# Kernel optimization log

Measured on AMD Instinct MI355X. Metric: run time of the kernel, lower is better.

## Reference

```python
import jax, jax.numpy as jnp
import numpy as np

DIM_CAP = 16   # capsule dim
NCLS = 17      # annotation_nr
BS = 16
T = 120        # chunk_size * fps
P = 22         # players per frame graph
G = BS * T     # number of graphs = 1920
N = G * P      # nodes = 42240
C_IN = 14
CHS = [16, 32, 64, 152]  # 8m,16m,32m,76m with m=2
BN_EPS = 1e-3


def _build_graph():
    # fully-connected directed edges within each 22-node graph (no self loops)
    ii, jj = np.meshgrid(np.arange(P), np.arange(P), indexing='ij')
    mask = ii != jj
    li, lj = ii[mask], jj[mask]               # (462,)
    base = (np.arange(G) * P)[:, None]
    src = (base + li[None, :]).reshape(-1)
    dst = (base + lj[None, :]).reshape(-1)
    edge_index = np.stack([src, dst]).astype(np.int64)   # (2, E)
    batch = np.repeat(np.arange(G), P).astype(np.int64)  # (N,)
    return jnp.asarray(edge_index), jnp.asarray(batch)


def setup_inputs() -> dict:
    key = jax.random.key(0)
    ks = jax.random.split(key, 16)
    edge_index, batch = _build_graph()
    E = edge_index.shape[1]
    x = jax.random.normal(ks[0], (N, C_IN), dtype=jnp.float32)
    edge_attr = jax.random.uniform(ks[1], (E, 5), dtype=jnp.float32)
    dims = [C_IN] + CHS
    params = {}
    for i in range(4):
        s = 1.0 / np.sqrt(dims[i])
        params[f'W{i+1}'] = jax.random.normal(ks[2 + i], (dims[i], dims[i + 1]), dtype=jnp.float32) * s
        params[f'b{i+1}'] = jnp.zeros((dims[i + 1],), dtype=jnp.float32)
    c_out = DIM_CAP * NCLS  # 272
    params['conv_w'] = jax.random.normal(ks[6], (c_out, CHS[-1], 3), dtype=jnp.float32) * (1.0 / np.sqrt(CHS[-1] * 3))
    params['conv_b'] = jnp.zeros((c_out,), dtype=jnp.float32)
    params['bn_gamma'] = jnp.ones((T,), dtype=jnp.float32)
    params['bn_beta'] = jnp.zeros((T,), dtype=jnp.float32)
    return dict(x=x, edge_index=edge_index, batch=batch, edge_attr=edge_attr, **params)


def _gcn_layer(x, src, dst, w_edge, W, b):
    # PyG GCNConv: x' = D^-1/2 (A + I) D^-1/2 (x W) + b, edge weights w, self-loop weight 1
    n = x.shape[0]
    h = x @ W
    loop = jnp.arange(n)
    src_f = jnp.concatenate([src, loop])
    dst_f = jnp.concatenate([dst, loop])
    w_f = jnp.concatenate([w_edge, jnp.ones((n,), h.dtype)])
    deg = jax.ops.segment_sum(w_f, dst_f, num_segments=n)
    dinv = jnp.where(deg > 0, jax.lax.rsqrt(deg), 0.0)
    norm = dinv[src_f] * w_f * dinv[dst_f]
    out = jax.ops.segment_sum(norm[:, None] * h[src_f], dst_f, num_segments=n)
    return out + b


def reference(x, edge_index, batch, edge_attr, W1, b1, W2, b2, W3, b3, W4, b4,
              conv_w, conv_b, bn_gamma, bn_beta):
    src, dst = edge_index[0], edge_index[1]
    ew = edge_attr[:, 4]
    h = jax.nn.relu(_gcn_layer(x, src, dst, ew, W1, b1))
    h = jax.nn.relu(_gcn_layer(h, src, dst, ew, W2, b2))
    h = jax.nn.relu(_gcn_layer(h, src, dst, ew, W3, b3))
    h = jax.nn.relu(_gcn_layer(h, src, dst, ew, W4, b4))
    # global mean pool per graph -> (G, 152)
    ones = jnp.ones((h.shape[0],), h.dtype)
    cnt = jax.ops.segment_sum(ones, batch, num_segments=G)
    pooled = jax.ops.segment_sum(h, batch, num_segments=G) / jnp.clip(cnt, 1.0)[:, None]
    # (BS, T, 152) -> (BS, 152, T); conv kernel (3,1) with pad (1,1) on T
    feat = pooled.reshape(BS, T, CHS[-1]).transpose(0, 2, 1)
    conv = jax.lax.conv_general_dilated(
        feat, conv_w, window_strides=(1,), padding=[(1, 1)],
        dimension_numbers=('NCH', 'OIH', 'NCH'))
    conv = conv + conv_b[None, :, None]            # (BS, 272, T)
    caps = conv.transpose(0, 2, 1).reshape(BS, T, DIM_CAP, NCLS)
    # BatchNorm2d(num_features=T) in eval mode: running mean 0, var 1
    scale = (bn_gamma / jnp.sqrt(1.0 + BN_EPS))[None, :, None, None]
    shift = bn_beta[None, :, None, None]
    s = jax.nn.sigmoid(caps * scale + shift)
    out = jnp.sqrt(jnp.sum(jnp.square(s - 0.5), axis=2) * 4.0 / DIM_CAP)
    return out  # (BS, T, NCLS)
```

## Files before the change

### kernel.cpp

```cpp
#include <hip/hip_runtime.h>
#include <hip/hip_bf16.h>

#define GROUPS 1920
#define CH4 152
#define BUFS 100

template<int DIN, int KR>
__device__ __forceinline__ void layerA(const float* buf, float* Ut,
                                       const float* A4, int tid)
{
    constexpr int NKT = DIN / KR;
    constexpr int NT = NKT * 12;
    if (tid < NT) {
        const int kt = tid / 12, pt = tid - kt * 12;
        const int g = pt / 3, ps = (pt - g * 3) * 8;
        const int col0 = g * 24 + ps;
        const int xcol = g * 24;
        float acc[KR][8];
        #pragma unroll
        for (int j = 0; j < KR; ++j)
            #pragma unroll
            for (int a = 0; a < 8; ++a) acc[j][a] = 0.f;
        #pragma unroll 2
        for (int q = 0; q < 22; ++q) {
            const float4 a0 = *(const float4*)(A4 + (q * 4 + g) * 28 + ps);
            const float4 a1 = *(const float4*)(A4 + (q * 4 + g) * 28 + ps + 4);
            float xv[KR];
            #pragma unroll
            for (int j = 0; j < KR; ++j) xv[j] = buf[(kt * KR + j) * BUFS + xcol + q];
            #pragma unroll
            for (int j = 0; j < KR; ++j) {
                acc[j][0] = fmaf(xv[j], a0.x, acc[j][0]);
                acc[j][1] = fmaf(xv[j], a0.y, acc[j][1]);
                acc[j][2] = fmaf(xv[j], a0.z, acc[j][2]);
                acc[j][3] = fmaf(xv[j], a0.w, acc[j][3]);
                acc[j][4] = fmaf(xv[j], a1.x, acc[j][4]);
                acc[j][5] = fmaf(xv[j], a1.y, acc[j][5]);
                acc[j][6] = fmaf(xv[j], a1.z, acc[j][6]);
                acc[j][7] = fmaf(xv[j], a1.w, acc[j][7]);
            }
        }
        #pragma unroll
        for (int j = 0; j < KR; ++j) {
            *(float4*)(Ut + (kt * KR + j) * BUFS + col0) =
                make_float4(acc[j][0], acc[j][1], acc[j][2], acc[j][3]);
            *(float4*)(Ut + (kt * KR + j) * BUFS + col0 + 4) =
                make_float4(acc[j][4], acc[j][5], acc[j][6], acc[j][7]);
        }
    }
}

template<int DIN, int DOUT, int CR>
__device__ __forceinline__ void layerB(const float* __restrict__ W,
                                       const float* __restrict__ B,
                                       const float* Ut, float* buf, int tid)
{
    constexpr int NCT = DOUT / CR;
    constexpr int NT = NCT * 12;
    if (tid < NT) {
        const int ct = tid / 12, pt = tid - ct * 12;
        const int p0 = pt * 8, c0 = ct * CR;
        float acc[CR][8];
        #pragma unroll
        for (int b = 0; b < CR; ++b) {
            const float bias = B[c0 + b];
            #pragma unroll
            for (int a = 0; a < 8; ++a) acc[b][a] = bias;
        }
        #pragma unroll 4
        for (int k = 0; k < DIN; ++k) {
            const float4 u0 = *(const float4*)(Ut + k * BUFS + p0);
            const float4 u1 = *(const float4*)(Ut + k * BUFS + p0 + 4);
            float wv[CR];
            #pragma unroll
            for (int b = 0; b < CR; b += 4) {
                const float4 w4 = *(const float4*)(W + k * DOUT + c0 + b);
                wv[b] = w4.x; wv[b + 1] = w4.y; wv[b + 2] = w4.z; wv[b + 3] = w4.w;
            }
            #pragma unroll
            for (int b = 0; b < CR; ++b) {
                acc[b][0] = fmaf(wv[b], u0.x, acc[b][0]);
                acc[b][1] = fmaf(wv[b], u0.y, acc[b][1]);
                acc[b][2] = fmaf(wv[b], u0.z, acc[b][2]);
                acc[b][3] = fmaf(wv[b], u0.w, acc[b][3]);
                acc[b][4] = fmaf(wv[b], u1.x, acc[b][4]);
                acc[b][5] = fmaf(wv[b], u1.y, acc[b][5]);
                acc[b][6] = fmaf(wv[b], u1.z, acc[b][6]);
                acc[b][7] = fmaf(wv[b], u1.w, acc[b][7]);
            }
        }
        #pragma unroll
        for (int b = 0; b < CR; ++b) {
            *(float4*)(buf + (c0 + b) * BUFS + p0) =
                make_float4(fmaxf(acc[b][0], 0.f), fmaxf(acc[b][1], 0.f),
                            fmaxf(acc[b][2], 0.f), fmaxf(acc[b][3], 0.f));
            *(float4*)(buf + (c0 + b) * BUFS + p0 + 4) =
                make_float4(fmaxf(acc[b][4], 0.f), fmaxf(acc[b][5], 0.f),
                            fmaxf(acc[b][6], 0.f), fmaxf(acc[b][7], 0.f));
        }
    }
}

__global__ __launch_bounds__(256) void gcn_kernel(
    const float* __restrict__ x, const float* __restrict__ ea,
    const float* __restrict__ W1, const float* __restrict__ b1,
    const float* __restrict__ W2, const float* __restrict__ b2,
    const float* __restrict__ W3, const float* __restrict__ b3,
    const float* __restrict__ W4, const float* __restrict__ b4,
    float* __restrict__ pooledT)
{
    __shared__ __align__(16) float A4[24 * 4 * 28];
    __shared__ __align__(16) float dv[4 * 24];
    __shared__ __align__(16) float buf[64 * BUFS];
    __shared__ __align__(16) float Ut[64 * BUFS];

    const int tid = threadIdx.x;
    const int G0 = blockIdx.x * 4;

    for (int idx = tid; idx < 24 * 4 * 28; idx += 256) {
        const int q = idx / 112, r = idx - q * 112;
        const int g = r / 28, p = r - g * 28;
        float v = 0.f;
        if (q < 22 && p < 22) {
            if (q == p) v = 1.0f;
            else {
                const int e = q * 21 + p - (p > q);
                v = ea[((size_t)(G0 + g) * 462 + e) * 5 + 4];
            }
        }
        A4[idx] = v;
    }
    for (int idx = tid; idx < 14 * 96; idx += 256) {
        const int k = idx / 96, col = idx - k * 96;
        const int g = col / 24, p = col - g * 24;
        buf[k * BUFS + col] = (p < 22) ? x[((size_t)(G0 + g) * 22 + p) * 14 + k] : 0.f;
    }
    __syncthreads();

    if (tid < 96) {
        const int g = tid / 24, p = tid - g * 24;
        float s = 0.f;
        #pragma unroll
        for (int q = 0; q < 22; ++q) s += A4[(q * 4 + g) * 28 + p];
        dv[tid] = (s > 0.f) ? rsqrtf(s) : 0.f;
    }
    __syncthreads();
    for (int idx = tid; idx < 24 * 4 * 28; idx += 256) {
        const int q = idx / 112, r = idx - q * 112;
        const int g = r / 28, p = r - g * 28;
        if (p < 24) A4[idx] *= dv[g * 24 + q] * dv[g * 24 + p];
    }
    __syncthreads();

    layerA<14, 2>(buf, Ut, A4, tid);  __syncthreads();
    layerB<14, 16, 4>(W1, b1, Ut, buf, tid);  __syncthreads();
    layerA<16, 4>(buf, Ut, A4, tid);  __syncthreads();
    layerB<16, 32, 4>(W2, b2, Ut, buf, tid);  __syncthreads();
    layerA<32, 4>(buf, Ut, A4, tid);  __syncthreads();
    layerB<32, 64, 8>(W3, b3, Ut, buf, tid);  __syncthreads();
    layerA<64, 4>(buf, Ut, A4, tid);  __syncthreads();

    float* pscr = buf;
    if (tid < 19 * 12) {
        const int ct = tid / 12, pt = tid - ct * 12;
        const int p0 = pt * 8, c0 = ct * 8;
        float acc[8][8];
        #pragma unroll
        for (int b = 0; b < 8; ++b) {
            const float bias = b4[c0 + b];
            #pragma unroll
            for (int a = 0; a < 8; ++a) acc[b][a] = bias;
        }
        #pragma unroll 4
        for (int k = 0; k < 64; ++k) {
            const float4 u0 = *(const float4*)(Ut + k * BUFS + p0);
            const float4 u1 = *(const float4*)(Ut + k * BUFS + p0 + 4);
            float wv[8];
            #pragma unroll
            for (int b = 0; b < 8; b += 4) {
                const float4 w4 = *(const float4*)(W4 + k * 152 + c0 + b);
                wv[b] = w4.x; wv[b + 1] = w4.y; wv[b + 2] = w4.z; wv[b + 3] = w4.w;
            }
            #pragma unroll
            for (int b = 0; b < 8; ++b) {
                acc[b][0] = fmaf(wv[b], u0.x, acc[b][0]);
                acc[b][1] = fmaf(wv[b], u0.y, acc[b][1]);
                acc[b][2] = fmaf(wv[b], u0.z, acc[b][2]);
                acc[b][3] = fmaf(wv[b], u0.w, acc[b][3]);
                acc[b][4] = fmaf(wv[b], u1.x, acc[b][4]);
                acc[b][5] = fmaf(wv[b], u1.y, acc[b][5]);
                acc[b][6] = fmaf(wv[b], u1.z, acc[b][6]);
                acc[b][7] = fmaf(wv[b], u1.w, acc[b][7]);
            }
        }
        const int alim = ((pt % 3) == 2) ? 6 : 8;
        float ps8[8];
        #pragma unroll
        for (int b = 0; b < 8; ++b) {
            float s = 0.f;
            #pragma unroll
            for (int a = 0; a < 8; ++a)
                s += (a < alim) ? fmaxf(acc[b][a], 0.f) : 0.f;
            ps8[b] = s;
        }
        *(float4*)(pscr + pt * 152 + c0) = make_float4(ps8[0], ps8[1], ps8[2], ps8[3]);
        *(float4*)(pscr + pt * 152 + c0 + 4) = make_float4(ps8[4], ps8[5], ps8[6], ps8[7]);
    }
    __syncthreads();

    if (tid < 152) {
        const int c = tid;
        const int b = G0 / 120, t0 = G0 - b * 120;
        float4 v;
        #pragma unroll
        for (int g = 0; g < 4; ++g) {
            const float s = pscr[(g * 3 + 0) * 152 + c] + pscr[(g * 3 + 1) * 152 + c]
                          + pscr[(g * 3 + 2) * 152 + c];
            ((float*)&v)[g] = s * (1.0f / 22.0f);
        }
        *(float4*)(pooledT + ((size_t)(b * 152 + c) * 128) + 4 + t0) = v;
    }
}

__global__ __launch_bounds__(256) void repack_conv_w(const float* __restrict__ cw,
                                                     float* __restrict__ wT,
                                                     float* __restrict__ pT)
{
    const int idx = blockIdx.x * 256 + threadIdx.x;
    if (idx < 272 * 456) {
        const int o = idx / 456, r = idx - o * 456;
        wT[r * 272 + o] = cw[idx];
    } else {
        const int j = idx - 272 * 456;
        if (j < 16 * 152 * 8) {
            const int row = j >> 3, s = j & 7;
            const int slot = (s < 4) ? s : s + 120;
            pT[(size_t)row * 128 + slot] = 0.f;
        }
    }
}

__global__ __launch_bounds__(320) void conv_caps_kernel(
    const float* __restrict__ pT, const float* __restrict__ wT,
    const float* __restrict__ cb, const float* __restrict__ gamma,
    const float* __restrict__ beta, float* __restrict__ out)
{
    __shared__ __align__(16) float s2[8 * 272];
    __shared__ float sc[8], sh[8];

    const int bx = blockIdx.x;
    const int b = bx / 15, tile = bx - b * 15;
    const int t0 = tile * 8;
    const int tid = threadIdx.x;

    if (tid < 8) {
        const int t = t0 + tid;
        sc[tid] = gamma[t] * 0.999500374688f;
        sh[tid] = beta[t];
    }
    __syncthreads();

    if (tid < 272) {
        const int o = tid;
        const float cb0 = cb[o];
        float acc[8];
        #pragma unroll
        for (int tt = 0; tt < 8; ++tt) acc[tt] = cb0;
        const float* wp0 = wT + o;
        const float* frow0 = pT + ((size_t)b * 152) * 128 + 3 + t0;
        float w0 = wp0[0], w1 = wp0[272], w2 = wp0[544];
        #pragma unroll 2
        for (int i = 0; i < CH4; ++i) {
            const int inext = (i == CH4 - 1) ? i : i + 1;
            const float* nwp = wp0 + inext * 816;
            const float nw0 = nwp[0], nw1 = nwp[272], nw2 = nwp[544];
            const float* f = frow0 + (size_t)i * 128;
            float fr[10];
            #pragma unroll
            for (int j = 0; j < 10; ++j) fr[j] = f[j];
            #pragma unroll
            for (int tt = 0; tt < 8; ++tt)
                acc[tt] = fmaf(w0, fr[tt], fmaf(w1, fr[tt + 1], fmaf(w2, fr[tt + 2], acc[tt])));
            w0 = nw0; w1 = nw1; w2 = nw2;
        }
        #pragma unroll
        for (int tt = 0; tt < 8; ++tt) {
            const float z = fmaf(acc[tt], sc[tt], sh[tt]);
            const float s = 1.0f / (1.0f + __expf(-z));
            const float d = s - 0.5f;
            s2[tt * 272 + o] = d * d;
        }
    }
    __syncthreads();

    for (int e = tid; e < 8 * 17; e += 320) {
        const int tt = e / 17, n = e - tt * 17;
        float s = 0.f;
        #pragma unroll
        for (int d = 0; d < 16; ++d) s += s2[tt * 272 + d * 17 + n];
        out[((size_t)b * 120 + t0 + tt) * 17 + n] = sqrtf(s) * 0.5f;
    }
}

extern "C" void kernel_launch(void* const* d_in, const int* in_sizes, int n_in,
                              void* d_out, int out_size, void* d_ws, size_t ws_size,
                              hipStream_t stream) {
    const float* x     = (const float*)d_in[0];
    const float* ea    = (const float*)d_in[3];
    const float* W1    = (const float*)d_in[4];
    const float* b1    = (const float*)d_in[5];
    const float* W2    = (const float*)d_in[6];
    const float* b2    = (const float*)d_in[7];
    const float* W3    = (const float*)d_in[8];
    const float* b3    = (const float*)d_in[9];
    const float* W4    = (const float*)d_in[10];
    const float* b4    = (const float*)d_in[11];
    const float* cw    = (const float*)d_in[12];
    const float* cb    = (const float*)d_in[13];
    const float* gamma = (const float*)d_in[14];
    const float* beta  = (const float*)d_in[15];
    float* out = (float*)d_out;

    float* pT = (float*)d_ws;
    float* wT = pT + (size_t)16 * 152 * 128;

    hipLaunchKernelGGL(repack_conv_w, dim3((272 * 456 + 16 * 152 * 8 + 255) / 256),
                       dim3(256), 0, stream, cw, wT, pT);
    hipLaunchKernelGGL(gcn_kernel, dim3(GROUPS / 4), dim3(256), 0, stream,
                       x, ea, W1, b1, W2, b2, W3, b3, W4, b4, pT);
    hipLaunchKernelGGL(conv_caps_kernel, dim3(16 * 15), dim3(320), 0, stream,
                       pT, wT, cb, gamma, beta, out);
}
```

Measured before the change: 168.9 us.

## Process one graph per 64-thread block with XOR-swizzled shared layout

The GCN kernel now handles one graph per block of 64 threads (1920 blocks) instead of four graphs per 256-thread block (480 blocks). Shared-memory tiles shrink to 32-wide rows with an XOR swizzle meant to avoid bank conflicts, and per-thread register tiles are retuned (smaller KR/CR). The aim is more blocks for better occupancy and load balance across CUs, fewer idle threads, and less LDS per block. The trade-offs are less reuse of weight loads across graphs, scalar rather than float4 pooled writes, and more launch and setup work spread over more blocks.

New measurement: 172.2 us. No clear change (+1.9%).

```diff
diff --git a/kernel.cpp b/kernel.cpp
--- a/kernel.cpp
+++ b/kernel.cpp
@@ -3,19 +3,23 @@
 
 #define GROUPS 1920
 #define CH4 152
-#define BUFS 100
+
+__device__ __forceinline__ int rh(int r) { return (r + (r >> 3)) & 7; }
+__device__ __forceinline__ int swz(int r, int c) {
+    return (r << 5) + ((((c >> 2) ^ rh(r)) << 2) | (c & 3));
+}
+__device__ __forceinline__ int swz4(int r, int c4) {
+    return (r << 5) + ((c4 ^ rh(r)) << 2);
+}
 
 template<int DIN, int KR>
 __device__ __forceinline__ void layerA(const float* buf, float* Ut,
-                                       const float* A4, int tid)
-{
-    constexpr int NKT = DIN / KR;
-    constexpr int NT = NKT * 12;
+                                       const float* A, int tid)
+{
+    constexpr int NT = (DIN / KR) * 3;
     if (tid < NT) {
-        const int kt = tid / 12, pt = tid - kt * 12;
-        const int g = pt / 3, ps = (pt - g * 3) * 8;
-        const int col0 = g * 24 + ps;
-        const int xcol = g * 24;
+        const int kt = tid / 3, pt = tid - kt * 3;
+        const int p0 = pt * 8;
         float acc[KR][8];
         #pragma unroll
         for (int j = 0; j < KR; ++j)
@@ -23,11 +27,11 @@
             for (int a = 0; a < 8; ++a) acc[j][a] = 0.f;
         #pragma unroll 2
         for (int q = 0; q < 22; ++q) {
-            const float4 a0 = *(const float4*)(A4 + (q * 4 + g) * 28 + ps);
-            const float4 a1 = *(const float4*)(A4 + (q * 4 + g) * 28 + ps + 4);
+            const float4 a0 = *(const float4*)(A + q * 28 + p0);
+            const float4 a1 = *(const float4*)(A + q * 28 + p0 + 4);
             float xv[KR];
             #pragma unroll
-            for (int j = 0; j < KR; ++j) xv[j] = buf[(kt * KR + j) * BUFS + xcol + q];
+            for (int j = 0; j < KR; ++j) xv[j] = buf[swz(kt * KR + j, q)];
             #pragma unroll
             for (int j = 0; j < KR; ++j) {
                 acc[j][0] = fmaf(xv[j], a0.x, acc[j][0]);
@@ -42,9 +46,10 @@
         }
         #pragma unroll
         for (int j = 0; j < KR; ++j) {
-            *(float4*)(Ut + (kt * KR + j) * BUFS + col0) =
+            const int k = kt * KR + j;
+            *(float4*)(Ut + swz4(k, pt * 2)) =
                 make_float4(acc[j][0], acc[j][1], acc[j][2], acc[j][3]);
-            *(float4*)(Ut + (kt * KR + j) * BUFS + col0 + 4) =
+            *(float4*)(Ut + swz4(k, pt * 2 + 1)) =
                 make_float4(acc[j][4], acc[j][5], acc[j][6], acc[j][7]);
         }
     }
@@ -52,30 +57,36 @@
 
 template<int DIN, int DOUT, int CR>
 __device__ __forceinline__ void layerB(const float* __restrict__ W,
-                                       const float* __restrict__ B,
+                                       const float* __restrict__ Bb,
                                        const float* Ut, float* buf, int tid)
 {
-    constexpr int NCT = DOUT / CR;
-    constexpr int NT = NCT * 12;
+    constexpr int NT = (DOUT / CR) * 3;
     if (tid < NT) {
-        const int ct = tid / 12, pt = tid - ct * 12;
-        const int p0 = pt * 8, c0 = ct * CR;
+        const int ct = tid / 3, pt = tid - ct * 3;
+        const int c0 = ct * CR;
         float acc[CR][8];
         #pragma unroll
         for (int b = 0; b < CR; ++b) {
-            const float bias = B[c0 + b];
+            const float bias = Bb[c0 + b];
             #pragma unroll
             for (int a = 0; a < 8; ++a) acc[b][a] = bias;
         }
-        #pragma unroll 4
+        #pragma unroll 2
         for (int k = 0; k < DIN; ++k) {
-            const float4 u0 = *(const float4*)(Ut + k * BUFS + p0);
-            const float4 u1 = *(const float4*)(Ut + k * BUFS + p0 + 4);
+            const float4 u0 = *(const float4*)(Ut + swz4(k, pt * 2));
+            const float4 u1 = *(const float4*)(Ut + swz4(k, pt * 2 + 1));
             float wv[CR];
-            #pragma unroll
-            for (int b = 0; b < CR; b += 4) {
-                const float4 w4 = *(const float4*)(W + k * DOUT + c0 + b);
-                wv[b] = w4.x; wv[b + 1] = w4.y; wv[b + 2] = w4.z; wv[b + 3] = w4.w;
+            if constexpr (CR == 1) {
+                wv[0] = W[k * DOUT + c0];
+            } else if constexpr (CR == 2) {
+                const float2 w2 = *(const float2*)(W + k * DOUT + c0);
+                wv[0] = w2.x; wv[1] = w2.y;
+            } else {
+                #pragma unroll
+                for (int b = 0; b < CR; b += 4) {
+                    const float4 w4 = *(const float4*)(W + k * DOUT + c0 + b);
+                    wv[b] = w4.x; wv[b + 1] = w4.y; wv[b + 2] = w4.z; wv[b + 3] = w4.w;
+                }
             }
             #pragma unroll
             for (int b = 0; b < CR; ++b) {
@@ -91,17 +102,18 @@
         }
         #pragma unroll
         for (int b = 0; b < CR; ++b) {
-            *(float4*)(buf + (c0 + b) * BUFS + p0) =
+            const int r = c0 + b;
+            *(float4*)(buf + swz4(r, pt * 2)) =
                 make_float4(fmaxf(acc[b][0], 0.f), fmaxf(acc[b][1], 0.f),
                             fmaxf(acc[b][2], 0.f), fmaxf(acc[b][3], 0.f));
-            *(float4*)(buf + (c0 + b) * BUFS + p0 + 4) =
+            *(float4*)(buf + swz4(r, pt * 2 + 1)) =
                 make_float4(fmaxf(acc[b][4], 0.f), fmaxf(acc[b][5], 0.f),
                             fmaxf(acc[b][6], 0.f), fmaxf(acc[b][7], 0.f));
         }
     }
 }
 
-__global__ __launch_bounds__(256) void gcn_kernel(
+__global__ __launch_bounds__(64) void gcn_kernel(
     const float* __restrict__ x, const float* __restrict__ ea,
     const float* __restrict__ W1, const float* __restrict__ b1,
     const float* __restrict__ W2, const float* __restrict__ b2,
@@ -109,61 +121,58 @@
     const float* __restrict__ W4, const float* __restrict__ b4,
     float* __restrict__ pooledT)
 {
-    __shared__ __align__(16) float A4[24 * 4 * 28];
-    __shared__ __align__(16) float dv[4 * 24];
-    __shared__ __align__(16) float buf[64 * BUFS];
-    __shared__ __align__(16) float Ut[64 * BUFS];
+    __shared__ __align__(16) float sA[24 * 28];
+    __shared__ float dv[24];
+    __shared__ __align__(16) float buf[64 * 32];
+    __shared__ __align__(16) float Ut[64 * 32];
 
     const int tid = threadIdx.x;
-    const int G0 = blockIdx.x * 4;
-
-    for (int idx = tid; idx < 24 * 4 * 28; idx += 256) {
-        const int q = idx / 112, r = idx - q * 112;
-        const int g = r / 28, p = r - g * 28;
+    const int g = blockIdx.x;
+
+    for (int idx = tid; idx < 24 * 28; idx += 64) {
+        const int q = idx / 28, p = idx - q * 28;
         float v = 0.f;
         if (q < 22 && p < 22) {
             if (q == p) v = 1.0f;
             else {
                 const int e = q * 21 + p - (p > q);
-                v = ea[((size_t)(G0 + g) * 462 + e) * 5 + 4];
-            }
-        }
-        A4[idx] = v;
-    }
-    for (int idx = tid; idx < 14 * 96; idx += 256) {
-        const int k = idx / 96, col = idx - k * 96;
-        const int g = col / 24, p = col - g * 24;
-        buf[k * BUFS + col] = (p < 22) ? x[((size_t)(G0 + g) * 22 + p) * 14 + k] : 0.f;
-    }
-    __syncthreads();
-
-    if (tid < 96) {
-        const int g = tid / 24, p = tid - g * 24;
+                v = ea[((size_t)g * 462 + e) * 5 + 4];
+            }
+        }
+        sA[idx] = v;
+    }
+    for (int idx = tid; idx < 14 * 24; idx += 64) {
+        const int k = idx / 24, p = idx - k * 24;
+        buf[swz(k, p)] = (p < 22) ? x[((size_t)g * 22 + p) * 14 + k] : 0.f;
+    }
+    __syncthreads();
+
+    if (tid < 24) {
+        const int p = tid;
         float s = 0.f;
         #pragma unroll
-        for (int q = 0; q < 22; ++q) s += A4[(q * 4 + g) * 28 + p];
-        dv[tid] = (s > 0.f) ? rsqrtf(s) : 0.f;
-    }
-    __syncthreads();
-    for (int idx = tid; idx < 24 * 4 * 28; idx += 256) {
-        const int q = idx / 112, r = idx - q * 112;
-        const int g = r / 28, p = r - g * 28;
-        if (p < 24) A4[idx] *= dv[g * 24 + q] * dv[g * 24 + p];
-    }
-    __syncthreads();
-
-    layerA<14, 2>(buf, Ut, A4, tid);  __syncthreads();
-    layerB<14, 16, 4>(W1, b1, Ut, buf, tid);  __syncthreads();
-    layerA<16, 4>(buf, Ut, A4, tid);  __syncthreads();
-    layerB<16, 32, 4>(W2, b2, Ut, buf, tid);  __syncthreads();
-    layerA<32, 4>(buf, Ut, A4, tid);  __syncthreads();
-    layerB<32, 64, 8>(W3, b3, Ut, buf, tid);  __syncthreads();
-    layerA<64, 4>(buf, Ut, A4, tid);  __syncthreads();
-
-    float* pscr = buf;
-    if (tid < 19 * 12) {
-        const int ct = tid / 12, pt = tid - ct * 12;
-        const int p0 = pt * 8, c0 = ct * 8;
+        for (int q = 0; q < 22; ++q) s += sA[q * 28 + p];
+        dv[p] = (s > 0.f) ? rsqrtf(s) : 0.f;
+    }
+    __syncthreads();
+    for (int idx = tid; idx < 24 * 28; idx += 64) {
+        const int q = idx / 28, p = idx - q * 28;
+        if (p < 24) sA[idx] *= dv[q] * dv[p];
+    }
+    __syncthreads();
+
+    layerA<14, 1>(buf, Ut, sA, tid);           __syncthreads();
+    layerB<14, 16, 1>(W1, b1, Ut, buf, tid);   __syncthreads();
+    layerA<16, 1>(buf, Ut, sA, tid);           __syncthreads();
+    layerB<16, 32, 2>(W2, b2, Ut, buf, tid);   __syncthreads();
+    layerA<32, 2>(buf, Ut, sA, tid);           __syncthreads();
+    layerB<32, 64, 4>(W3, b3, Ut, buf, tid);   __syncthreads();
+    layerA<64, 4>(buf, Ut, sA, tid);           __syncthreads();
+
+    float* pscr = sA;
+    if (tid < 19 * 3) {
+        const int ct = tid / 3, pt = tid - ct * 3;
+        const int c0 = ct * 8;
         float acc[8][8];
         #pragma unroll
         for (int b = 0; b < 8; ++b) {
@@ -171,10 +180,10 @@
             #pragma unroll
             for (int a = 0; a < 8; ++a) acc[b][a] = bias;
         }
-        #pragma unroll 4
+        #pragma unroll 2
         for (int k = 0; k < 64; ++k) {
-            const float4 u0 = *(const float4*)(Ut + k * BUFS + p0);
-            const float4 u1 = *(const float4*)(Ut + k * BUFS + p0 + 4);
+            const float4 u0 = *(const float4*)(Ut + swz4(k, pt * 2));
+            const float4 u1 = *(const float4*)(Ut + swz4(k, pt * 2 + 1));
             float wv[8];
             #pragma unroll
             for (int b = 0; b < 8; b += 4) {
@@ -193,32 +202,27 @@
                 acc[b][7] = fmaf(wv[b], u1.w, acc[b][7]);
             }
         }
-        const int alim = ((pt % 3) == 2) ? 6 : 8;
-        float ps8[8];
+        const int alim = (pt == 2) ? 6 : 8;
+        float ps[8];
         #pragma unroll
         for (int b = 0; b < 8; ++b) {
             float s = 0.f;
             #pragma unroll
             for (int a = 0; a < 8; ++a)
                 s += (a < alim) ? fmaxf(acc[b][a], 0.f) : 0.f;
-            ps8[b] = s;
-        }
-        *(float4*)(pscr + pt * 152 + c0) = make_float4(ps8[0], ps8[1], ps8[2], ps8[3]);
-        *(float4*)(pscr + pt * 152 + c0 + 4) = make_float4(ps8[4], ps8[5], ps8[6], ps8[7]);
-    }
-    __syncthreads();
-
-    if (tid < 152) {
-        const int c = tid;
-        const int b = G0 / 120, t0 = G0 - b * 120;
-        float4 v;
-        #pragma unroll
-        for (int g = 0; g < 4; ++g) {
-            const float s = pscr[(g * 3 + 0) * 152 + c] + pscr[(g * 3 + 1) * 152 + c]
-                          + pscr[(g * 3 + 2) * 152 + c];
-            ((float*)&v)[g] = s * (1.0f / 22.0f);
-        }
-        *(float4*)(pooledT + ((size_t)(b * 152 + c) * 128) + 4 + t0) = v;
+            ps[b] = s;
+        }
+        *(float4*)(pscr + pt * 152 + c0)     = make_float4(ps[0], ps[1], ps[2], ps[3]);
+        *(float4*)(pscr + pt * 152 + c0 + 4) = make_float4(ps[4], ps[5], ps[6], ps[7]);
+    }
+    __syncthreads();
+
+    {
+        const int b = g / 120, t = g - b * 120;
+        for (int c = tid; c < 152; c += 64) {
+            const float s = pscr[c] + pscr[152 + c] + pscr[304 + c];
+            pooledT[(((size_t)(b * 152 + c)) << 7) + 4 + t] = s * (1.0f / 22.0f);
+        }
     }
 }
 
@@ -326,7 +330,7 @@
 
     hipLaunchKernelGGL(repack_conv_w, dim3((272 * 456 + 16 * 152 * 8 + 255) / 256),
                        dim3(256), 0, stream, cw, wT, pT);
-    hipLaunchKernelGGL(gcn_kernel, dim3(GROUPS / 4), dim3(256), 0, stream,
+    hipLaunchKernelGGL(gcn_kernel, dim3(GROUPS), dim3(64), 0, stream,
                        x, ea, W1, b1, W2, b2, W3, b3, W4, b4, pT);
     hipLaunchKernelGGL(conv_caps_kernel, dim3(16 * 15), dim3(320), 0, stream,
                        pT, wT, cb, gamma, beta, out);
```
